# Kernel optimization log

Hardware: AMD Instinct MI355X
Metric: run time of the kernel (lower is better)

Reference implementation:

```python
import jax, jax.numpy as jnp
import numpy as np

BS, Q, K, NT = 16, 1500, 256, 150   # batch, queries, classes, GT per image (T = BS*NT)
COST_CLASS, COST_BBOX, COST_GIOU = 1.0, 5.0, 2.0
ALPHA, GAMMA, EPS = 0.25, 2.0, 1e-8


def box_cxcywh_to_xyxy(b):
    cx, cy, w, h = b[..., 0], b[..., 1], b[..., 2], b[..., 3]
    return jnp.stack([cx - 0.5 * w, cy - 0.5 * h, cx + 0.5 * w, cy + 0.5 * h], axis=-1)


def generalized_box_iou(boxes1, boxes2):
    # boxes in xyxy; boxes1: [N,4], boxes2: [M,4] -> [N,M]
    area1 = (boxes1[:, 2] - boxes1[:, 0]) * (boxes1[:, 3] - boxes1[:, 1])
    area2 = (boxes2[:, 2] - boxes2[:, 0]) * (boxes2[:, 3] - boxes2[:, 1])
    lt = jnp.maximum(boxes1[:, None, :2], boxes2[None, :, :2])
    rb = jnp.minimum(boxes1[:, None, 2:], boxes2[None, :, 2:])
    wh = jnp.clip(rb - lt, 0.0)
    inter = wh[..., 0] * wh[..., 1]
    union = area1[:, None] + area2[None, :] - inter
    iou = inter / union
    # smallest enclosing box
    lt_e = jnp.minimum(boxes1[:, None, :2], boxes2[None, :, :2])
    rb_e = jnp.maximum(boxes1[:, None, 2:], boxes2[None, :, 2:])
    wh_e = jnp.clip(rb_e - lt_e, 0.0)
    area_e = wh_e[..., 0] * wh_e[..., 1]
    return iou - (area_e - union) / area_e


def setup_inputs() -> dict:
    key = jax.random.key(0)
    k1, k2, k3, k4 = jax.random.split(key, 4)
    pred_logits = jax.random.normal(k1, (BS, Q, K), dtype=jnp.float32)
    pred_boxes = jax.random.uniform(k2, (BS, Q, 4), dtype=jnp.float32, minval=0.05, maxval=0.95)
    tgt_bbox = jax.random.uniform(k3, (BS * NT, 4), dtype=jnp.float32, minval=0.05, maxval=0.95)
    tgt_ids = jax.random.randint(k4, (BS * NT,), 0, K)
    return {"pred_logits": pred_logits, "pred_boxes": pred_boxes,
            "tgt_bbox": tgt_bbox, "tgt_ids": tgt_ids}


def reference(pred_logits, pred_boxes, tgt_bbox, tgt_ids):
    bs, nq, k = pred_logits.shape
    out_prob = jax.nn.sigmoid(pred_logits.reshape(bs * nq, k))   # [N, K]
    out_bbox = pred_boxes.reshape(bs * nq, 4)                    # [N, 4]

    # focal-style classification cost, gathered at target class columns
    neg_cost = (1.0 - ALPHA) * out_prob ** GAMMA * -jnp.log(1.0 - out_prob + EPS)
    pos_cost = ALPHA * (1.0 - out_prob) ** GAMMA * -jnp.log(out_prob + EPS)
    cost_class = (pos_cost - neg_cost)[:, tgt_ids]               # [N, T]

    # L1 box cost (cdist p=1)
    cost_bbox = jnp.sum(jnp.abs(out_bbox[:, None, :] - tgt_bbox[None, :, :]), axis=-1)

    # negative GIoU cost
    cost_giou = -generalized_box_iou(box_cxcywh_to_xyxy(out_bbox),
                                     box_cxcywh_to_xyxy(tgt_bbox))

    C = COST_BBOX * cost_bbox + COST_CLASS * cost_class + COST_GIOU * cost_giou
    return C.reshape(bs, nq, -1)                                  # [bs, Q, T]
```

## Files before the change

### kernel.cpp

```cpp
#include <hip/hip_runtime.h>
#include <hip/hip_fp16.h>
#include <cmath>


namespace {
constexpr int kBS = 16, kQ = 1500, kK = 256, kNT = 150;
constexpr int kT  = kBS * kNT;
constexpr int kN  = kBS * kQ;
constexpr int kQB = 16;
constexpr int kTT = 1024;
constexpr int kTiles = 3;
constexpr float kAlpha = 0.25f;
constexpr float kEps   = 1e-8f;
}

__global__ __launch_bounds__(256, 4)
void matcher_cost_kernel(const float* __restrict__ logits,
                         const float* __restrict__ pboxes,
                         const float* __restrict__ tboxes,
                         const int*   __restrict__ tids,
                         float* __restrict__ out)
{
    __shared__ float2 s_cxy[kTT];
    __shared__ float2 s_wh[kTT];
    __shared__ unsigned char s_cid[kTT];
    __shared__ __half s_fcl[kQB][kK];

    const int tid  = threadIdx.x;
    const int n0   = blockIdx.x * kQB;
    const int t0   = blockIdx.y * kTT;
    const int tsz  = min(kTT, kT - t0);

    const float4* tb4 = reinterpret_cast<const float4*>(tboxes);
    for (int j = tid; j < tsz; j += 256) {
        const float4 b = tb4[t0 + j];
        s_cxy[j] = make_float2(b.x, b.y);
        s_wh[j]  = make_float2(b.z, b.w);
        s_cid[j] = (unsigned char)tids[t0 + j];
    }

    for (int q = 0; q < kQB; ++q) {
        const float x   = logits[(n0 + q) * kK + tid];
        const float p   = __builtin_amdgcn_rcpf(1.0f + __expf(-x));
        const float omp = 1.0f - p;
        const float cc  = -kAlpha * omp * omp * __logf(p + kEps)
                        + (1.0f - kAlpha) * p * p * __logf(omp + kEps);
        s_fcl[q][tid] = __float2half(cc);
    }

    __syncthreads();

    for (int q = 0; q < kQB; ++q) {
        const int n = n0 + q;
        const float pcx = pboxes[n * 4 + 0];
        const float pcy = pboxes[n * 4 + 1];
        const float pw  = pboxes[n * 4 + 2];
        const float ph  = pboxes[n * 4 + 3];
        const float px1 = pcx - 0.5f * pw, px2 = pcx + 0.5f * pw;
        const float py1 = pcy - 0.5f * ph, py2 = pcy + 0.5f * ph;
        const float parea = pw * ph;
        float* __restrict__ row = out + (size_t)n * kT + t0;

        auto body = [&](int t) {
            const float2 cxy = s_cxy[t];
            const float2 wh  = s_wh[t];
            const float bcx = cxy.x, bcy = cxy.y, bw = wh.x, bh = wh.y;
            const float cc = __half2float(s_fcl[q][s_cid[t]]);
            const float cb = fabsf(pcx - bcx) + fabsf(pcy - bcy)
                           + fabsf(pw - bw)  + fabsf(ph - bh);
            const float tx1 = bcx - 0.5f * bw, tx2 = bcx + 0.5f * bw;
            const float ty1 = bcy - 0.5f * bh, ty2 = bcy + 0.5f * bh;
            const float ow = fminf(px2, tx2) - fmaxf(px1, tx1);
            const float oh = fminf(py2, ty2) - fmaxf(py1, ty1);
            const float iw = fmaxf(ow, 0.0f), ih = fmaxf(oh, 0.0f);
            const float ew = (pw + bw) - ow,  eh = (ph + bh) - oh;
            const float inter = iw * ih;
            const float uni   = parea + bw * bh - inter;
            const float earea = ew * eh;
            const float r    = __builtin_amdgcn_rcpf(uni * earea);
            const float frac = fmaf(uni, uni, inter * earea) * r;
            row[t] = fmaf(5.0f, cb, cc + 2.0f) - 2.0f * frac;
        };

        if (tsz == kTT) {
#pragma unroll
            for (int e = 0; e < 4; ++e) body(tid + 256 * e);
        } else {
            for (int t = tid; t < tsz; t += 256) body(t);
        }
    }
}

extern "C" void kernel_launch(void* const* d_in, const int* in_sizes, int n_in,
                              void* d_out, int out_size, void* d_ws, size_t ws_size,
                              hipStream_t stream) {
    const float* logits = (const float*)d_in[0];
    const float* pboxes = (const float*)d_in[1];
    const float* tboxes = (const float*)d_in[2];
    const int*   tids   = (const int*)d_in[3];
    float* out = (float*)d_out;

    dim3 grid(kN / kQB, kTiles);
    dim3 block(256);
    hipLaunchKernelGGL(matcher_cost_kernel, grid, block, 0, stream,
                       logits, pboxes, tboxes, tids, out);
}
```

Baseline: 274.7 us.

## Register-block target boxes and tile queries by four with fp32 class-cost table

Each thread now loads its four target boxes once into registers and precomputes their corners and areas. It then processes queries in groups of four, so per-target geometry is reused across queries. The class-cost table becomes fp32, transposed to [class][query] with a stride of 20, which lets one float4 LDS read fetch four queries' costs, and the fp16 conversion is dropped. This raises register pressure and LDS use (about 20KB for the table), which may cut occupancy under launch_bounds(256,4); the kernel is store-bound, so the gain may be limited.

Measured after the change: 276.4 us. No clear change (+0.6%).

```diff
diff --git a/kernel.cpp b/kernel.cpp
--- a/kernel.cpp
+++ b/kernel.cpp
@@ -1,5 +1,4 @@
 #include <hip/hip_runtime.h>
-#include <hip/hip_fp16.h>
 #include <cmath>
 
 
@@ -10,6 +9,7 @@
 constexpr int kQB = 16;
 constexpr int kTT = 1024;
 constexpr int kTiles = 3;
+constexpr int kFS = 20;
 constexpr float kAlpha = 0.25f;
 constexpr float kEps   = 1e-8f;
 }
@@ -21,72 +21,89 @@
                          const int*   __restrict__ tids,
                          float* __restrict__ out)
 {
-    __shared__ float2 s_cxy[kTT];
-    __shared__ float2 s_wh[kTT];
+    __shared__ float4 s_box[kTT];
     __shared__ unsigned char s_cid[kTT];
-    __shared__ __half s_fcl[kQB][kK];
+    __shared__ float s_fcl[kK * kFS];
 
-    const int tid  = threadIdx.x;
-    const int n0   = blockIdx.x * kQB;
-    const int t0   = blockIdx.y * kTT;
-    const int tsz  = min(kTT, kT - t0);
+    const int tid = threadIdx.x;
+    const int n0  = blockIdx.x * kQB;
+    const int t0  = blockIdx.y * kTT;
+    const int tsz = min(kTT, kT - t0);
 
     const float4* tb4 = reinterpret_cast<const float4*>(tboxes);
     for (int j = tid; j < tsz; j += 256) {
-        const float4 b = tb4[t0 + j];
-        s_cxy[j] = make_float2(b.x, b.y);
-        s_wh[j]  = make_float2(b.z, b.w);
+        s_box[j] = tb4[t0 + j];
         s_cid[j] = (unsigned char)tids[t0 + j];
     }
 
+#pragma unroll
     for (int q = 0; q < kQB; ++q) {
-        const float x   = logits[(n0 + q) * kK + tid];
+        const float x   = logits[(size_t)(n0 + q) * kK + tid];
         const float p   = __builtin_amdgcn_rcpf(1.0f + __expf(-x));
         const float omp = 1.0f - p;
         const float cc  = -kAlpha * omp * omp * __logf(p + kEps)
                         + (1.0f - kAlpha) * p * p * __logf(omp + kEps);
-        s_fcl[q][tid] = __float2half(cc);
+        s_fcl[tid * kFS + q] = cc;
+    }
+    __syncthreads();
+
+    float bcx[4], bcy[4], bwv[4], bhv[4];
+    float tx1[4], tx2[4], ty1[4], ty2[4], barea[4];
+    int   cofs[4];
+    bool  act[4];
+#pragma unroll
+    for (int g = 0; g < 4; ++g) {
+        const int t = tid + 256 * g;
+        act[g] = (t < tsz);
+        if (256 * g < tsz) {
+            const float4 b = s_box[t];
+            bcx[g] = b.x; bcy[g] = b.y; bwv[g] = b.z; bhv[g] = b.w;
+            tx1[g] = b.x - 0.5f * b.z;  tx2[g] = b.x + 0.5f * b.z;
+            ty1[g] = b.y - 0.5f * b.w;  ty2[g] = b.y + 0.5f * b.w;
+            barea[g] = b.z * b.w;
+            cofs[g] = (int)s_cid[t] * kFS;
+        }
     }
 
-    __syncthreads();
+    for (int qt = 0; qt < 4; ++qt) {
+        float pcx[4], pcy[4], pw[4], ph[4];
+        float px1[4], px2[4], py1[4], py2[4], parea[4];
+#pragma unroll
+        for (int qq = 0; qq < 4; ++qq) {
+            const int n = n0 + qt * 4 + qq;
+            pcx[qq] = pboxes[n * 4 + 0];
+            pcy[qq] = pboxes[n * 4 + 1];
+            pw[qq]  = pboxes[n * 4 + 2];
+            ph[qq]  = pboxes[n * 4 + 3];
+            px1[qq] = pcx[qq] - 0.5f * pw[qq];  px2[qq] = pcx[qq] + 0.5f * pw[qq];
+            py1[qq] = pcy[qq] - 0.5f * ph[qq];  py2[qq] = pcy[qq] + 0.5f * ph[qq];
+            parea[qq] = pw[qq] * ph[qq];
+        }
+        float* __restrict__ base = out + (size_t)(n0 + qt * 4) * kT + t0;
 
-    for (int q = 0; q < kQB; ++q) {
-        const int n = n0 + q;
-        const float pcx = pboxes[n * 4 + 0];
-        const float pcy = pboxes[n * 4 + 1];
-        const float pw  = pboxes[n * 4 + 2];
-        const float ph  = pboxes[n * 4 + 3];
-        const float px1 = pcx - 0.5f * pw, px2 = pcx + 0.5f * pw;
-        const float py1 = pcy - 0.5f * ph, py2 = pcy + 0.5f * ph;
-        const float parea = pw * ph;
-        float* __restrict__ row = out + (size_t)n * kT + t0;
-
-        auto body = [&](int t) {
-            const float2 cxy = s_cxy[t];
-            const float2 wh  = s_wh[t];
-            const float bcx = cxy.x, bcy = cxy.y, bw = wh.x, bh = wh.y;
-            const float cc = __half2float(s_fcl[q][s_cid[t]]);
-            const float cb = fabsf(pcx - bcx) + fabsf(pcy - bcy)
-                           + fabsf(pw - bw)  + fabsf(ph - bh);
-            const float tx1 = bcx - 0.5f * bw, tx2 = bcx + 0.5f * bw;
-            const float ty1 = bcy - 0.5f * bh, ty2 = bcy + 0.5f * bh;
-            const float ow = fminf(px2, tx2) - fmaxf(px1, tx1);
-            const float oh = fminf(py2, ty2) - fmaxf(py1, ty1);
-            const float iw = fmaxf(ow, 0.0f), ih = fmaxf(oh, 0.0f);
-            const float ew = (pw + bw) - ow,  eh = (ph + bh) - oh;
-            const float inter = iw * ih;
-            const float uni   = parea + bw * bh - inter;
-            const float earea = ew * eh;
-            const float r    = __builtin_amdgcn_rcpf(uni * earea);
-            const float frac = fmaf(uni, uni, inter * earea) * r;
-            row[t] = fmaf(5.0f, cb, cc + 2.0f) - 2.0f * frac;
-        };
-
-        if (tsz == kTT) {
 #pragma unroll
-            for (int e = 0; e < 4; ++e) body(tid + 256 * e);
-        } else {
-            for (int t = tid; t < tsz; t += 256) body(t);
+        for (int g = 0; g < 4; ++g) {
+            if (256 * g >= tsz) continue;
+            const float4 f4 =
+                *reinterpret_cast<const float4*>(&s_fcl[cofs[g] + qt * 4]);
+            const float fc[4] = {f4.x, f4.y, f4.z, f4.w};
+#pragma unroll
+            for (int qq = 0; qq < 4; ++qq) {
+                const float cb = fabsf(pcx[qq] - bcx[g]) + fabsf(pcy[qq] - bcy[g])
+                               + fabsf(pw[qq] - bwv[g]) + fabsf(ph[qq] - bhv[g]);
+                const float ow = fminf(px2[qq], tx2[g]) - fmaxf(px1[qq], tx1[g]);
+                const float oh = fminf(py2[qq], ty2[g]) - fmaxf(py1[qq], ty1[g]);
+                const float iw = fmaxf(ow, 0.0f), ih = fmaxf(oh, 0.0f);
+                const float ew = pw[qq] + bwv[g] - ow;
+                const float eh = ph[qq] + bhv[g] - oh;
+                const float inter = iw * ih;
+                const float uni   = parea[qq] + barea[g] - inter;
+                const float earea = ew * eh;
+                const float r    = __builtin_amdgcn_rcpf(uni * earea);
+                const float frac = fmaf(uni, uni, inter * earea) * r;
+                const float v    = fmaf(5.0f, cb, fc[qq] + 2.0f) - 2.0f * frac;
+                if (act[g]) base[(size_t)qq * kT + 256 * g + tid] = v;
+            }
         }
     }
 }
```
